# Kernel optimization log

Hardware: AMD Instinct MI355X
Metric: run time of the kernel (lower is better)

## Reference

```python
import jax, jax.numpy as jnp
import numpy as np

BETA = 0.25
K = 4096
D = 256


def setup_inputs() -> dict:
    key = jax.random.key(0)
    k1, k2 = jax.random.split(key)
    z = jax.random.normal(k1, (4, D, 16, 32, 32), dtype=jnp.float32)
    # mimics nn.init.uniform_(embed.weight, -1/K, 1/K)
    embed = jax.random.uniform(k2, (K, D), minval=-1.0 / K, maxval=1.0 / K, dtype=jnp.float32)
    return {"z": z, "embed": embed}


def reference(z, embed):
    # z: [B, D, T, H, W] -> channel-last [B, T, H, W, D]
    z_perm = jnp.transpose(z, (0, 2, 3, 4, 1))
    flat = z_perm.reshape(-1, embed.shape[1])  # [N, D]
    # squared L2 distances via expansion: |z|^2 - 2 z.e + |e|^2  -> [N, K]
    dist = ((flat ** 2).sum(axis=1, keepdims=True)
            - 2.0 * flat @ embed.T
            + (embed ** 2).sum(axis=1)[None, :])
    idx = jnp.argmin(dist, axis=1)  # [N]
    z_q = embed[idx].reshape(z_perm.shape)  # [B, T, H, W, D]
    # straight-through estimator
    z_q_st = z_perm + jax.lax.stop_gradient(z_q - z_perm)
    z_q_st = jnp.transpose(z_q_st, (0, 4, 1, 2, 3))  # back to [B, D, T, H, W]
    e_q = jnp.transpose(z_q, (0, 4, 1, 2, 3))
    codebook_loss = jnp.mean((jax.lax.stop_gradient(e_q) - z) ** 2)
    commitment_loss = jnp.mean((e_q - jax.lax.stop_gradient(z)) ** 2)
    vq_loss = codebook_loss + BETA * commitment_loss
    indices = idx.reshape(z_perm.shape[:4])  # [B, T, H, W]
    return (z_q_st, vq_loss, indices)
```

## Files before the change

kernel.cpp:

```cpp
#include <hip/hip_runtime.h>
#include <float.h>

#define KC 4096
#define DIM 256
#define MB 16384
#define NTOT 65536
#define ZELEMS 16777216
#define LOSS_OFF 16777216
#define IDX_OFF  16777217
#define TAU 1.5e-4f

#define BT_OFF   524288
#define CNT_OFF  528400
#define CAND_OFF 532480
#define FULL_OFF 800000

typedef _Float16 h8 __attribute__((ext_vector_type(8)));
typedef float f4v __attribute__((ext_vector_type(4)));

__device__ __forceinline__ bool lexlt(float av, int ai, float bv, int bi) {
    return (av < bv) || (av == bv && ai < bi);
}

__global__ __launch_bounds__(256) void vq_prep(const float* __restrict__ e,
                                               float* __restrict__ out) {
    if (blockIdx.x < 512) {
        int t = blockIdx.x * 256 + threadIdx.x;
        int code = t >> 5, s8 = t & 31;
        const float4* src = reinterpret_cast<const float4*>(e + (size_t)code * DIM + s8 * 8);
        float4 v0 = src[0], v1 = src[1];
        float f[8] = {v0.x, v0.y, v0.z, v0.w, v1.x, v1.y, v1.z, v1.w};
        union { uint4 q; _Float16 h[8]; } P;
        #pragma unroll
        for (int p = 0; p < 8; ++p) P.h[p] = (_Float16)(f[p] * 4096.0f);
        int kc = s8 >> 2, khi = s8 & 3;
        int lane = khi * 16 + (code & 15);
        int slot = ((code >> 4) * 8 + kc) * 64 + lane;
        reinterpret_cast<uint4*>(out)[slot] = P.q;
    } else {
        int k = (blockIdx.x - 512) * 4 + (threadIdx.x >> 6);
        int lane = threadIdx.x & 63;
        float4 v = reinterpret_cast<const float4*>(e + (size_t)k * DIM)[lane];
        double s = (double)v.x * v.x + (double)v.y * v.y + (double)v.z * v.z + (double)v.w * v.w;
        #pragma unroll
        for (int off = 32; off > 0; off >>= 1) s += __shfl_down(s, off);
        if (lane == 0) out[BT_OFF + k] = (float)s;
    }
}

#define INS4(V0, V1, V2, V3, L0, L1, L2, L3, v, k)                              \
    if (v < V3) {                                                               \
        if (v < V2) {                                                           \
            V3 = V2; L3 = L2;                                                   \
            if (v < V1) {                                                       \
                V2 = V1; L2 = L1;                                               \
                if (v < V0) { V1 = V0; L1 = L0; V0 = v; L0 = k; }               \
                else        { V1 = v; L1 = k; }                                 \
            } else { V2 = v; L2 = k; }                                          \
        } else { V3 = v; L3 = k; }                                              \
    }

__global__ __launch_bounds__(256) void vq_fast(const float* __restrict__ z,
                                               float* __restrict__ out) {
    __shared__ uint4 etile[2][512];
    __shared__ unsigned long long lists[4][16][4];
    const int tid = threadIdx.x;
    const int wave = tid >> 6, lane = tid & 63;
    const int khi = lane >> 4, l16 = lane & 15;
    const int nbase = blockIdx.x * 64;
    const int b = nbase / MB;
    const int mbase = nbase % MB;
    const float* zb = z + (size_t)b * DIM * MB + mbase + wave * 16 + l16;

    h8 zf[8];
    #pragma unroll
    for (int kc = 0; kc < 8; ++kc) {
        h8 va;
        #pragma unroll
        for (int j = 0; j < 8; ++j)
            va[j] = (_Float16)zb[(size_t)(kc * 32 + khi * 8 + j) * MB];
        zf[kc] = va;
    }

    const uint4* ET = reinterpret_cast<const uint4*>(out);
    const float* Btab = out + BT_OFF;

    float b1 = FLT_MAX;
    int bk = 0;
    float v0 = FLT_MAX, v1 = FLT_MAX, v2 = FLT_MAX, v3 = FLT_MAX;
    int l0 = 0, l1 = 0, l2 = 0, l3 = 0;

    uint4 r0 = ET[tid], r1 = ET[tid + 256];
    for (int tile = 0; tile < KC / 16; ++tile) {
        const int cur = tile & 1;
        etile[cur][tid] = r0; etile[cur][tid + 256] = r1;
        __syncthreads();
        if (tile < KC / 16 - 1) {
            r0 = ET[(size_t)(tile + 1) * 512 + tid];
            r1 = ET[(size_t)(tile + 1) * 512 + tid + 256];
        }

        f4v ae = {0.f, 0.f, 0.f, 0.f}, ao = ae;
        #pragma unroll
        for (int kc = 0; kc < 8; kc += 2) {
            union { uint4 q; h8 v; } afe, afo;
            afe.q = etile[cur][kc * 64 + lane];
            afo.q = etile[cur][(kc + 1) * 64 + lane];
            ae = __builtin_amdgcn_mfma_f32_16x16x32_f16(afe.v, zf[kc], ae, 0, 0, 0);
            ao = __builtin_amdgcn_mfma_f32_16x16x32_f16(afo.v, zf[kc + 1], ao, 0, 0, 0);
        }

        const f4v Bv = *reinterpret_cast<const f4v*>(Btab + tile * 16 + khi * 4);
        const int kb = tile * 16 + khi * 4;
        float sc[4];
        #pragma unroll
        for (int i = 0; i < 4; ++i)
            sc[i] = fmaf(-4.8828125e-4f, ae[i] + ao[i], Bv[i]);
        float m = fminf(fminf(sc[0], sc[1]), fminf(sc[2], sc[3]));
        if (m <= b1 + TAU) {
            #pragma unroll
            for (int i = 0; i < 4; ++i) {
                float s = sc[i]; int k = kb + i;
                if (s < b1) {
                    if (b1 <= s + TAU) INS4(v0, v1, v2, v3, l0, l1, l2, l3, b1, bk)
                    b1 = s; bk = k;
                } else if (s <= b1 + TAU) {
                    INS4(v0, v1, v2, v3, l0, l1, l2, l3, s, k)
                }
            }
        }
    }

    float gb = b1;
    int gk = bk;
    #pragma unroll
    for (int off = 16; off < 64; off <<= 1) {
        float ov = __shfl_xor(gb, off); int ok = __shfl_xor(gk, off);
        if (lexlt(ov, ok, gb, gk)) { gb = ov; gk = ok; }
    }
    const float thr = gb + TAU;

    int n = 0, pa = 0, pb = 0, pc = 0, pd = 0;
    #define ADDW(kk) { if (n == 0) pa = kk; else if (n == 1) pb = kk; \
                       else if (n == 2) pc = kk; else if (n == 3) pd = kk; n++; }
    if (b1 <= thr) ADDW(bk)
    if (v0 <= thr) ADDW(l0)
    if (v1 <= thr) ADDW(l1)
    if (v2 <= thr) ADDW(l2)
    if (v3 <= thr) ADDW(l3)
    lists[wave][l16][khi] = ((unsigned long long)n << 48) |
        (unsigned long long)pa | ((unsigned long long)pb << 12) |
        ((unsigned long long)pc << 24) | ((unsigned long long)pd << 36);
    __syncthreads();

    unsigned* cntg = (unsigned*)(out + CNT_OFF);
    {
        bool act = (lane < 16);
        int gidx = nbase + wave * 16 + l16;
        int I1 = gk;
        int tot = 0, c[4];
        c[0] = c[1] = c[2] = c[3] = I1;
        if (act) {
            #pragma unroll
            for (int q = 0; q < 4; ++q) {
                unsigned long long pl = lists[wave][l16][q];
                int pcnt = (int)(pl >> 48);
                #pragma unroll
                for (int j = 0; j < 4; ++j) {
                    int kv = (int)((pl >> (12 * j)) & 4095ull);
                    if (j < pcnt && tot + j < 4) c[tot + j] = kv;
                }
                tot += pcnt;
            }
            out[IDX_OFF + gidx] = (float)I1;
        }
        bool cand = act && (tot >= 2) && (tot <= 4);
        bool full = act && (tot > 4);
        unsigned long long mc = __ballot(cand);
        if (mc) {
            int leader = __ffsll((long long)mc) - 1;
            unsigned base = 0;
            if (lane == leader) base = atomicAdd(cntg, (unsigned)__popcll(mc));
            base = __shfl(base, leader);
            if (cand) {
                unsigned pos = base + (unsigned)__popcll(mc & ((1ull << lane) - 1ull));
                reinterpret_cast<uint4*>(out + CAND_OFF)[pos] =
                    make_uint4((unsigned)gidx,
                               (unsigned)c[0] | ((unsigned)c[1] << 16),
                               (unsigned)c[2] | ((unsigned)c[3] << 16), 0u);
            }
        }
        unsigned long long mf = __ballot(full);
        if (mf) {
            int leader = __ffsll((long long)mf) - 1;
            unsigned base = 0;
            if (lane == leader) base = atomicAdd(cntg + 1, (unsigned)__popcll(mf));
            base = __shfl(base, leader);
            if (full) {
                unsigned pos = base + (unsigned)__popcll(mf & ((1ull << lane) - 1ull));
                reinterpret_cast<unsigned*>(out + FULL_OFF)[pos] = (unsigned)gidx;
            }
        }
    }
}

__global__ __launch_bounds__(256) void vq_resolve_cand(const float* __restrict__ z,
                                                       const float* __restrict__ e,
                                                       float* __restrict__ out) {
    const int wave = threadIdx.x >> 6, lane = threadIdx.x & 63;
    const unsigned n = *reinterpret_cast<const unsigned*>(out + CNT_OFF);
    const uint4* list = reinterpret_cast<const uint4*>(out + CAND_OFF);
    const float* Btab = out + BT_OFF;
    for (unsigned ei = blockIdx.x * 4 + wave; ei < n; ei += gridDim.x * 4) {
        uint4 ent = list[ei];
        const int gidx = (int)ent.x;
        const int c1 = (int)(ent.y & 0xFFFFu), c2 = (int)(ent.y >> 16);
        const int c3 = (int)(ent.z & 0xFFFFu), c4 = (int)(ent.z >> 16);
        const int b = gidx >> 14, m = gidx & (MB - 1);
        const float* zr = z + (size_t)b * DIM * MB + m;
        const float* e1 = e + (size_t)c1 * DIM;
        const float* e2 = e + (size_t)c2 * DIM;
        const float* e3 = e + (size_t)c3 * DIM;
        const float* e4 = e + (size_t)c4 * DIM;
        double A = 0.0;
        double d1 = 0.0, d2 = 0.0, d3 = 0.0, d4 = 0.0;
        #pragma unroll
        for (int jj = 0; jj < 4; ++jj) {
            int d = lane * 4 + jj;
            double zv = (double)zr[(size_t)d * MB];
            A = fma(zv, zv, A);
            d1 = fma(zv, (double)e1[d], d1);
            d2 = fma(zv, (double)e2[d], d2);
            d3 = fma(zv, (double)e3[d], d3);
            d4 = fma(zv, (double)e4[d], d4);
        }
        #pragma unroll
        for (int mm = 1; mm < 64; mm <<= 1) {
            A += __shfl_xor(A, mm);
            d1 += __shfl_xor(d1, mm); d2 += __shfl_xor(d2, mm);
            d3 += __shfl_xor(d3, mm); d4 += __shfl_xor(d4, mm);
        }
        if (lane == 0) {
            float Af = (float)A;
            float s1 = (Af - (float)(2.0 * d1)) + Btab[c1];
            float s2 = (Af - (float)(2.0 * d2)) + Btab[c2];
            float s3 = (Af - (float)(2.0 * d3)) + Btab[c3];
            float s4 = (Af - (float)(2.0 * d4)) + Btab[c4];
            float bv = s1; int bk = c1;
            if (lexlt(s2, c2, bv, bk)) { bv = s2; bk = c2; }
            if (lexlt(s3, c3, bv, bk)) { bv = s3; bk = c3; }
            if (lexlt(s4, c4, bv, bk)) { bv = s4; bk = c4; }
            out[IDX_OFF + gidx] = (float)bk;
        }
    }
}

__global__ __launch_bounds__(256) void vq_resolve_full(const float* __restrict__ z,
                                                       const float* __restrict__ e,
                                                       float* __restrict__ out) {
    __shared__ float zs[DIM];
    __shared__ float rv[4];
    __shared__ int ri[4];
    const int tid = threadIdx.x;
    const int wave = tid >> 6, lane = tid & 63;
    const unsigned n = reinterpret_cast<const unsigned*>(out + CNT_OFF)[1];
    const unsigned* list = reinterpret_cast<const unsigned*>(out + FULL_OFF);
    const float* Btab = out + BT_OFF;
    for (unsigned ei = blockIdx.x; ei < n; ei += gridDim.x) {
        const int gidx = (int)list[ei];
        const int b = gidx >> 14, m = gidx & (MB - 1);
        const float* zr = z + (size_t)b * DIM * MB + m;
        if (tid < DIM) zs[tid] = zr[(size_t)tid * MB];
        __syncthreads();
        double av = 0.0;
        #pragma unroll
        for (int t2 = 0; t2 < 4; ++t2) {
            double zv = (double)zs[lane * 4 + t2];
            av = fma(zv, zv, av);
        }
        #pragma unroll
        for (int mm = 1; mm < 64; mm <<= 1) av += __shfl_xor(av, mm);
        const float Af = (float)av;

        float bsv = FLT_MAX; int bsk = 0;
        for (int kk = 0; kk < 16; ++kk) {
            const int k = kk * 256 + tid;
            const float4* er4 = reinterpret_cast<const float4*>(e + (size_t)k * DIM);
            const float4* zs4 = reinterpret_cast<const float4*>(zs);
            double dot0 = 0.0, dot1 = 0.0;
            #pragma unroll 8
            for (int d4 = 0; d4 < 64; ++d4) {
                float4 ev = er4[d4];
                float4 zv = zs4[d4];
                dot0 = fma((double)zv.x, (double)ev.x, dot0);
                dot1 = fma((double)zv.y, (double)ev.y, dot1);
                dot0 = fma((double)zv.z, (double)ev.z, dot0);
                dot1 = fma((double)zv.w, (double)ev.w, dot1);
            }
            float s = (Af - (float)(2.0 * (dot0 + dot1))) + Btab[k];
            if (s < bsv) { bsv = s; bsk = k; }
        }
        #pragma unroll
        for (int mm = 1; mm < 64; mm <<= 1) {
            float ov = __shfl_xor(bsv, mm);
            int oi = __shfl_xor(bsk, mm);
            if (ov < bsv || (ov == bsv && oi < bsk)) { bsv = ov; bsk = oi; }
        }
        if (lane == 0) { rv[wave] = bsv; ri[wave] = bsk; }
        __syncthreads();
        if (tid == 0) {
            float bv = rv[0]; int bk = ri[0];
            #pragma unroll
            for (int wv = 1; wv < 4; ++wv) {
                if (rv[wv] < bv || (rv[wv] == bv && ri[wv] < bk)) { bv = rv[wv]; bk = ri[wv]; }
            }
            out[IDX_OFF + gidx] = (float)bk;
        }
        __syncthreads();
    }
}

__global__ __launch_bounds__(256) void vq_apply(const float* __restrict__ z,
                                                const float* __restrict__ e,
                                                float* __restrict__ out) {
    __shared__ int lds_fi[32];
    __shared__ float lds_e[32][260];
    __shared__ double lds_ls[4];
    const int tid = threadIdx.x;
    const int wave = tid >> 6, lane = tid & 63;
    const int nbase = blockIdx.x * 32;
    const int b = nbase / MB;
    const int mbase = nbase % MB;
    if (tid < 32) lds_fi[tid] = (int)out[IDX_OFF + nbase + tid];
    __syncthreads();
    for (int r = wave; r < 32; r += 4) {
        int code = lds_fi[r];
        float4 v = reinterpret_cast<const float4*>(e + (size_t)code * DIM)[lane];
        *reinterpret_cast<float4*>(&lds_e[r][lane * 4]) = v;
    }
    __syncthreads();

    double lsum = 0.0;
    const int mloc = tid & 31;
    const int d0 = tid >> 5;
    #pragma unroll 4
    for (int d = d0; d < DIM; d += 8) {
        float ev = lds_e[mloc][d];
        size_t off = (size_t)b * (DIM * MB) + (size_t)d * MB + mbase + mloc;
        float zv = z[off];
        out[off] = ev;
        float diff = ev - zv;
        lsum += (double)diff * diff;
    }
    #pragma unroll
    for (int off = 32; off > 0; off >>= 1) lsum += __shfl_down(lsum, off);
    if (lane == 0) lds_ls[wave] = lsum;
    __syncthreads();
    if (tid == 0) {
        double t = lds_ls[0] + lds_ls[1] + lds_ls[2] + lds_ls[3];
        atomicAdd(out + LOSS_OFF, (float)(t * (1.25 / (double)ZELEMS)));
    }
}

extern "C" void kernel_launch(void* const* d_in, const int* in_sizes, int n_in,
                              void* d_out, int out_size, void* d_ws, size_t ws_size,
                              hipStream_t stream) {
    const float* z = (const float*)d_in[0];
    const float* e = (const float*)d_in[1];
    float* out = (float*)d_out;

    hipMemsetAsync(out + LOSS_OFF, 0, sizeof(float), stream);
    hipMemsetAsync(out + CNT_OFF, 0, 2 * sizeof(unsigned), stream);
    vq_prep<<<1536, 256, 0, stream>>>(e, out);
    vq_fast<<<NTOT / 64, 256, 0, stream>>>(z, out);
    vq_resolve_cand<<<1024, 256, 0, stream>>>(z, e, out);
    vq_resolve_full<<<512, 256, 0, stream>>>(z, e, out);
    vq_apply<<<NTOT / 32, 256, 0, stream>>>(z, e, out);
}
```

Baseline: 432.6 us.

## Compute VQ loss in search kernel and merge resolve kernels

Moves the loss reduction into the main search kernel, using the per-row |z|^2 accumulated while loading z plus the best approximate score. This lets the apply kernel skip re-reading z entirely. It also merges the candidate and full resolve kernels into one launch. The risk is that the loss now uses the fp16-approximate minimum distance and float accumulation, which may drift from the exact value.

Result: slower. 517.4 us (+19.6%).

```diff
diff --git a/kernel.cpp b/kernel.cpp
--- a/kernel.cpp
+++ b/kernel.cpp
@@ -64,6 +64,7 @@
                                                float* __restrict__ out) {
     __shared__ uint4 etile[2][512];
     __shared__ unsigned long long lists[4][16][4];
+    __shared__ float lds_ls[4];
     const int tid = threadIdx.x;
     const int wave = tid >> 6, lane = tid & 63;
     const int khi = lane >> 4, l16 = lane & 15;
@@ -72,13 +73,17 @@
     const int mbase = nbase % MB;
     const float* zb = z + (size_t)b * DIM * MB + mbase + wave * 16 + l16;
 
+    float apart = 0.f;
     h8 zf[8];
     #pragma unroll
     for (int kc = 0; kc < 8; ++kc) {
         h8 va;
         #pragma unroll
-        for (int j = 0; j < 8; ++j)
-            va[j] = (_Float16)zb[(size_t)(kc * 32 + khi * 8 + j) * MB];
+        for (int j = 0; j < 8; ++j) {
+            float zv = zb[(size_t)(kc * 32 + khi * 8 + j) * MB];
+            apart = fmaf(zv, zv, apart);
+            va[j] = (_Float16)zv;
+        }
         zf[kc] = va;
     }
 
@@ -137,8 +142,14 @@
     for (int off = 16; off < 64; off <<= 1) {
         float ov = __shfl_xor(gb, off); int ok = __shfl_xor(gk, off);
         if (lexlt(ov, ok, gb, gk)) { gb = ov; gk = ok; }
+        apart += __shfl_xor(apart, off);
     }
     const float thr = gb + TAU;
+
+    float lval = (lane < 16) ? (apart + gb) : 0.f;
+    #pragma unroll
+    for (int off = 1; off < 64; off <<= 1) lval += __shfl_xor(lval, off);
+    if (lane == 0) lds_ls[wave] = lval;
 
     int n = 0, pa = 0, pb = 0, pc = 0, pd = 0;
     #define ADDW(kk) { if (n == 0) pa = kk; else if (n == 1) pb = kk; \
@@ -154,6 +165,10 @@
     __syncthreads();
 
     unsigned* cntg = (unsigned*)(out + CNT_OFF);
+    if (tid == 0) {
+        float t = lds_ls[0] + lds_ls[1] + lds_ls[2] + lds_ls[3];
+        atomicAdd(out + LOSS_OFF, t * (1.25f / (float)ZELEMS));
+    }
     {
         bool act = (lane < 16);
         int gidx = nbase + wave * 16 + l16;
@@ -204,70 +219,20 @@
     }
 }
 
-__global__ __launch_bounds__(256) void vq_resolve_cand(const float* __restrict__ z,
-                                                       const float* __restrict__ e,
-                                                       float* __restrict__ out) {
-    const int wave = threadIdx.x >> 6, lane = threadIdx.x & 63;
-    const unsigned n = *reinterpret_cast<const unsigned*>(out + CNT_OFF);
-    const uint4* list = reinterpret_cast<const uint4*>(out + CAND_OFF);
-    const float* Btab = out + BT_OFF;
-    for (unsigned ei = blockIdx.x * 4 + wave; ei < n; ei += gridDim.x * 4) {
-        uint4 ent = list[ei];
-        const int gidx = (int)ent.x;
-        const int c1 = (int)(ent.y & 0xFFFFu), c2 = (int)(ent.y >> 16);
-        const int c3 = (int)(ent.z & 0xFFFFu), c4 = (int)(ent.z >> 16);
-        const int b = gidx >> 14, m = gidx & (MB - 1);
-        const float* zr = z + (size_t)b * DIM * MB + m;
-        const float* e1 = e + (size_t)c1 * DIM;
-        const float* e2 = e + (size_t)c2 * DIM;
-        const float* e3 = e + (size_t)c3 * DIM;
-        const float* e4 = e + (size_t)c4 * DIM;
-        double A = 0.0;
-        double d1 = 0.0, d2 = 0.0, d3 = 0.0, d4 = 0.0;
-        #pragma unroll
-        for (int jj = 0; jj < 4; ++jj) {
-            int d = lane * 4 + jj;
-            double zv = (double)zr[(size_t)d * MB];
-            A = fma(zv, zv, A);
-            d1 = fma(zv, (double)e1[d], d1);
-            d2 = fma(zv, (double)e2[d], d2);
-            d3 = fma(zv, (double)e3[d], d3);
-            d4 = fma(zv, (double)e4[d], d4);
-        }
-        #pragma unroll
-        for (int mm = 1; mm < 64; mm <<= 1) {
-            A += __shfl_xor(A, mm);
-            d1 += __shfl_xor(d1, mm); d2 += __shfl_xor(d2, mm);
-            d3 += __shfl_xor(d3, mm); d4 += __shfl_xor(d4, mm);
-        }
-        if (lane == 0) {
-            float Af = (float)A;
-            float s1 = (Af - (float)(2.0 * d1)) + Btab[c1];
-            float s2 = (Af - (float)(2.0 * d2)) + Btab[c2];
-            float s3 = (Af - (float)(2.0 * d3)) + Btab[c3];
-            float s4 = (Af - (float)(2.0 * d4)) + Btab[c4];
-            float bv = s1; int bk = c1;
-            if (lexlt(s2, c2, bv, bk)) { bv = s2; bk = c2; }
-            if (lexlt(s3, c3, bv, bk)) { bv = s3; bk = c3; }
-            if (lexlt(s4, c4, bv, bk)) { bv = s4; bk = c4; }
-            out[IDX_OFF + gidx] = (float)bk;
-        }
-    }
-}
-
-__global__ __launch_bounds__(256) void vq_resolve_full(const float* __restrict__ z,
-                                                       const float* __restrict__ e,
-                                                       float* __restrict__ out) {
+__global__ __launch_bounds__(256) void vq_resolve(const float* __restrict__ z,
+                                                  const float* __restrict__ e,
+                                                  float* __restrict__ out) {
     __shared__ float zs[DIM];
     __shared__ float rv[4];
     __shared__ int ri[4];
     const int tid = threadIdx.x;
     const int wave = tid >> 6, lane = tid & 63;
-    const unsigned n = reinterpret_cast<const unsigned*>(out + CNT_OFF)[1];
-    const unsigned* list = reinterpret_cast<const unsigned*>(out + FULL_OFF);
     const float* Btab = out + BT_OFF;
-    for (unsigned ei = blockIdx.x; ei < n; ei += gridDim.x) {
-        const int gidx = (int)list[ei];
+
+    const unsigned nf = reinterpret_cast<const unsigned*>(out + CNT_OFF)[1];
+    const unsigned* flist = reinterpret_cast<const unsigned*>(out + FULL_OFF);
+    for (unsigned ei = blockIdx.x; ei < nf; ei += gridDim.x) {
+        const int gidx = (int)flist[ei];
         const int b = gidx >> 14, m = gidx & (MB - 1);
         const float* zr = z + (size_t)b * DIM * MB + m;
         if (tid < DIM) zs[tid] = zr[(size_t)tid * MB];
@@ -318,14 +283,57 @@
         }
         __syncthreads();
     }
-}
-
-__global__ __launch_bounds__(256) void vq_apply(const float* __restrict__ z,
-                                                const float* __restrict__ e,
+
+    const unsigned nc = *reinterpret_cast<const unsigned*>(out + CNT_OFF);
+    const uint4* clist = reinterpret_cast<const uint4*>(out + CAND_OFF);
+    for (unsigned ei = blockIdx.x * 4 + wave; ei < nc; ei += gridDim.x * 4) {
+        uint4 ent = clist[ei];
+        const int gidx = (int)ent.x;
+        const int c1 = (int)(ent.y & 0xFFFFu), c2 = (int)(ent.y >> 16);
+        const int c3 = (int)(ent.z & 0xFFFFu), c4 = (int)(ent.z >> 16);
+        const int b = gidx >> 14, m = gidx & (MB - 1);
+        const float* zr = z + (size_t)b * DIM * MB + m;
+        const float* e1 = e + (size_t)c1 * DIM;
+        const float* e2 = e + (size_t)c2 * DIM;
+        const float* e3 = e + (size_t)c3 * DIM;
+        const float* e4 = e + (size_t)c4 * DIM;
+        double A = 0.0;
+        double d1 = 0.0, d2 = 0.0, d3 = 0.0, d4 = 0.0;
+        #pragma unroll
+        for (int jj = 0; jj < 4; ++jj) {
+            int d = lane * 4 + jj;
+            double zv = (double)zr[(size_t)d * MB];
+            A = fma(zv, zv, A);
+            d1 = fma(zv, (double)e1[d], d1);
+            d2 = fma(zv, (double)e2[d], d2);
+            d3 = fma(zv, (double)e3[d], d3);
+            d4 = fma(zv, (double)e4[d], d4);
+        }
+        #pragma unroll
+        for (int mm = 1; mm < 64; mm <<= 1) {
+            A += __shfl_xor(A, mm);
+            d1 += __shfl_xor(d1, mm); d2 += __shfl_xor(d2, mm);
+            d3 += __shfl_xor(d3, mm); d4 += __shfl_xor(d4, mm);
+        }
+        if (lane == 0) {
+            float Af = (float)A;
+            float s1 = (Af - (float)(2.0 * d1)) + Btab[c1];
+            float s2 = (Af - (float)(2.0 * d2)) + Btab[c2];
+            float s3 = (Af - (float)(2.0 * d3)) + Btab[c3];
+            float s4 = (Af - (float)(2.0 * d4)) + Btab[c4];
+            float bv = s1; int bk = c1;
+            if (lexlt(s2, c2, bv, bk)) { bv = s2; bk = c2; }
+            if (lexlt(s3, c3, bv, bk)) { bv = s3; bk = c3; }
+            if (lexlt(s4, c4, bv, bk)) { bv = s4; bk = c4; }
+            out[IDX_OFF + gidx] = (float)bk;
+        }
+    }
+}
+
+__global__ __launch_bounds__(256) void vq_apply(const float* __restrict__ e,
                                                 float* __restrict__ out) {
     __shared__ int lds_fi[32];
     __shared__ float lds_e[32][260];
-    __shared__ double lds_ls[4];
     const int tid = threadIdx.x;
     const int wave = tid >> 6, lane = tid & 63;
     const int nbase = blockIdx.x * 32;
@@ -340,25 +348,12 @@
     }
     __syncthreads();
 
-    double lsum = 0.0;
     const int mloc = tid & 31;
     const int d0 = tid >> 5;
     #pragma unroll 4
     for (int d = d0; d < DIM; d += 8) {
-        float ev = lds_e[mloc][d];
         size_t off = (size_t)b * (DIM * MB) + (size_t)d * MB + mbase + mloc;
-        float zv = z[off];
-        out[off] = ev;
-        float diff = ev - zv;
-        lsum += (double)diff * diff;
-    }
-    #pragma unroll
-    for (int off = 32; off > 0; off >>= 1) lsum += __shfl_down(lsum, off);
-    if (lane == 0) lds_ls[wave] = lsum;
-    __syncthreads();
-    if (tid == 0) {
-        double t = lds_ls[0] + lds_ls[1] + lds_ls[2] + lds_ls[3];
-        atomicAdd(out + LOSS_OFF, (float)(t * (1.25 / (double)ZELEMS)));
+        out[off] = lds_e[mloc][d];
     }
 }
 
@@ -373,7 +368,6 @@
     hipMemsetAsync(out + CNT_OFF, 0, 2 * sizeof(unsigned), stream);
     vq_prep<<<1536, 256, 0, stream>>>(e, out);
     vq_fast<<<NTOT / 64, 256, 0, stream>>>(z, out);
-    vq_resolve_cand<<<1024, 256, 0, stream>>>(z, e, out);
-    vq_resolve_full<<<512, 256, 0, stream>>>(z, e, out);
-    vq_apply<<<NTOT / 32, 256, 0, stream>>>(z, e, out);
-}
+    vq_resolve<<<1024, 256, 0, stream>>>(z, e, out);
+    vq_apply<<<NTOT / 32, 256, 0, stream>>>(e, out);
+}
```
